# Kernel tuning notes

Hardware: AMD Instinct MI355X
Metric: run time of the kernel (lower is better)

Reference implementation:

```python
import jax, jax.numpy as jnp
import numpy as np

THETA = 10000.0
MASK_FILL = -60000.0

def _rope(x):
    # lucidrains rotary_embedding_torch semantics: interleaved pairs, full-dim rotation
    S, D = x.shape[-2], x.shape[-1]
    inv_freq = 1.0 / (THETA ** (jnp.arange(0, D, 2, dtype=jnp.float32) / D))  # [D/2]
    freqs = jnp.arange(S, dtype=jnp.float32)[:, None] * inv_freq[None, :]     # [S, D/2]
    freqs = jnp.repeat(freqs, 2, axis=-1)                                     # [S, D] (each freq twice)
    cos, sin = jnp.cos(freqs), jnp.sin(freqs)
    xr = x.reshape(x.shape[:-1] + (D // 2, 2))
    rot_half = jnp.stack((-xr[..., 1], xr[..., 0]), axis=-1).reshape(x.shape)  # (x1,x2)->(-x2,x1)
    return x * cos + rot_half * sin

def setup_inputs() -> dict:
    key = jax.random.key(0)
    kq, kk, kv, km = jax.random.split(key, 4)
    B, H, S, D = 4, 16, 2048, 128
    return {
        "query": jax.random.normal(kq, (B, H, S, D), dtype=jnp.float32),
        "key": jax.random.normal(kk, (B, H, S, D), dtype=jnp.float32),
        "value": jax.random.normal(kv, (B, H, S, D), dtype=jnp.float32),
        "mask": jax.random.randint(km, (1, 1, S, S), 0, 2, dtype=jnp.int32),
    }

def reference(query, key, value, mask):
    q = _rope(query)
    k = _rope(key)
    scale = 1.0 / jnp.sqrt(jnp.float32(q.shape[-1]))
    scores = jnp.einsum('bhqd,bhkd->bhqk', q, k) * scale
    scores = jnp.where(mask == 0, jnp.float32(MASK_FILL), scores)
    p_attn = jax.nn.softmax(scores, axis=-1)
    out = jnp.einsum('bhqk,bhkd->bhqd', p_attn, value)
    return out, p_attn
```

## Files before the change

### kernel.cpp

```cpp
#include <hip/hip_runtime.h>
#include <hip/hip_fp16.h>
#include <cstdint>
#include <cstddef>

#define Bn 4
#define Hn 16
#define Sn 2048
#define Dn 128
#define MSHIFT 8.0f

typedef _Float16 half8  __attribute__((ext_vector_type(8)));
typedef float    f32x16 __attribute__((ext_vector_type(16)));
typedef float    f32x4v __attribute__((ext_vector_type(4)));
typedef unsigned uint4v __attribute__((ext_vector_type(4)));

__device__ __forceinline__ int pk_f16(float a, float b){
  auto h = __builtin_amdgcn_cvt_pkrtz(a, b);
  return __builtin_bit_cast(int, h);
}


__global__ void k_rope_table(float2* __restrict__ tab){
  const int idx = blockIdx.x*256 + threadIdx.x;
  const int i = idx & 63, s = idx >> 6;
  const double invf = exp(-(double)i * (9.210340371976184 / 64.0));
  const double ang  = (double)s * invf;
  float2 cs; cs.x = (float)cos(ang); cs.y = (float)sin(ang);
  tab[idx] = cs;
}

__global__ void k_pack_qk(const float* __restrict__ q, const float* __restrict__ k,
                          const float2* __restrict__ tab,
                          half8* __restrict__ qp, half8* __restrict__ kp){
  const int t    = blockIdx.x*256 + threadIdx.x;
  const int lane = t & 63, ln = lane & 31, h = lane >> 5;
  const int dc   = (t >> 6) & 7;
  const int blk  = (t >> 9) & 63;
  const int bh   = t >> 15;
  const int s    = blk*32 + ln;
  const size_t roff = ((size_t)bh*Sn + s)*Dn + dc*16 + h*8;
  const float4 a0 = *(const float4*)(q + roff);
  const float4 a1 = *(const float4*)(q + roff + 4);
  const float4 b0 = *(const float4*)(k + roff);
  const float4 b1 = *(const float4*)(k + roff + 4);
  const float2* tb = tab + s*64 + dc*8 + h*4;
  const float2 c0 = tb[0], c1 = tb[1], c2 = tb[2], c3 = tb[3];
  const float SC = 0.08838834764831845f;
  half8 qo, ko;
  qo[0] = (_Float16)((a0.x*c0.x - a0.y*c0.y)*SC);
  qo[1] = (_Float16)((a0.y*c0.x + a0.x*c0.y)*SC);
  qo[2] = (_Float16)((a0.z*c1.x - a0.w*c1.y)*SC);
  qo[3] = (_Float16)((a0.w*c1.x + a0.z*c1.y)*SC);
  qo[4] = (_Float16)((a1.x*c2.x - a1.y*c2.y)*SC);
  qo[5] = (_Float16)((a1.y*c2.x + a1.x*c2.y)*SC);
  qo[6] = (_Float16)((a1.z*c3.x - a1.w*c3.y)*SC);
  qo[7] = (_Float16)((a1.w*c3.x + a1.z*c3.y)*SC);
  ko[0] = (_Float16)(b0.x*c0.x - b0.y*c0.y);
  ko[1] = (_Float16)(b0.y*c0.x + b0.x*c0.y);
  ko[2] = (_Float16)(b0.z*c1.x - b0.w*c1.y);
  ko[3] = (_Float16)(b0.w*c1.x + b0.z*c1.y);
  ko[4] = (_Float16)(b1.x*c2.x - b1.y*c2.y);
  ko[5] = (_Float16)(b1.y*c2.x + b1.x*c2.y);
  ko[6] = (_Float16)(b1.z*c3.x - b1.w*c3.y);
  ko[7] = (_Float16)(b1.w*c3.x + b1.z*c3.y);
  qp[t] = qo;
  kp[t] = ko;
}

__global__ void k_pack_v(const float* __restrict__ v, half8* __restrict__ vp){
  const int t    = blockIdx.x*256 + threadIdx.x;
  const int lane = t & 63, ln = lane & 31, h = lane >> 5;
  const int dt   = (t >> 6) & 3;
  const int k16  = (t >> 8) & 127;
  const int bh   = t >> 15;
  const size_t base = ((size_t)bh*Sn + k16*16 + h*8)*Dn + dt*32 + ln;
  half8 o;
#pragma unroll
  for (int j = 0; j < 8; ++j) o[j] = (_Float16)v[base + (size_t)j*Dn];
  vp[t] = o;
}

__global__ void k_maskbits(const int* __restrict__ mask, unsigned* __restrict__ mtb){
  const int g = blockIdx.x*256 + threadIdx.x;
  const int k = g & (Sn-1), q32 = g >> 11;
  unsigned bits = 0u;
  for (int j = 0; j < 32; ++j)
    bits |= (mask[(size_t)(q32*32 + j)*Sn + k] != 0 ? 1u : 0u) << j;
  mtb[g] = bits;
}


__global__ __launch_bounds__(512, 2) void attn_ps2(
    const half8* __restrict__ qp, const half8* __restrict__ kp,
    const unsigned* __restrict__ mtb, half8* __restrict__ wfrag,
    float* __restrict__ rinvb)
{
  const int bid  = blockIdx.x;
  const int work = ((bid & 7) << 6) + (bid >> 3);
  const int bh   = work >> 3;
  const int qg   = work & 7;
  const int w    = threadIdx.x >> 6;
  const int l    = threadIdx.x & 63;
  const int ln   = l & 31;
  const int h    = l >> 5;
  const int qb   = qg*8 + w;
  const int strip = bh*64 + qb;

  half8 qf[8];
#pragma unroll
  for (int dc = 0; dc < 8; ++dc)
    qf[dc] = qp[(((size_t)bh*64 + qb)*8 + dc)*64 + l];

  const unsigned* mrow = mtb + (size_t)qb*Sn;
  half8* wbase = wfrag + (size_t)strip*128*64;
  float L = 0.f;

  for (int kt = 0; kt < 64; ++kt){
    const half8* kf = kp + (((size_t)bh*64 + kt)*8)*64 + l;
    f32x16 a;
#pragma unroll
    for (int i = 0; i < 16; ++i) a[i] = 0.f;
#pragma unroll
    for (int dc = 0; dc < 8; ++dc)
      a = __builtin_amdgcn_mfma_f32_32x32x16_f16(kf[(size_t)dc*64], qf[dc], a, 0, 0, 0);

#pragma unroll
    for (int mm = 0; mm < 4; ++mm){
      const uint4v dw = *(const uint4v*)(mrow + kt*32 + mm*8 + h*4);
#pragma unroll
      for (int aa = 0; aa < 4; ++aa){
        const int r = mm*4 + aa;
        const float s = ((dw[aa] >> ln) & 1u) ? a[r] : -1.0e30f;
        const float u = __expf(s - MSHIFT);
        a[r] = u;
        L += u;
      }
    }

    int pk2[4][2];
#pragma unroll
    for (int b = 0; b < 4; ++b){
      pk2[b][0] = pk_f16(a[4*b+0], a[4*b+1]);
      pk2[b][1] = pk_f16(a[4*b+2], a[4*b+3]);
    }

#pragma unroll
    for (int t16 = 0; t16 < 2; ++t16){
      const int P00 = pk2[2*t16+0][0];
      const int P01 = pk2[2*t16+0][1];
      const int P10 = pk2[2*t16+1][0];
      const int P11 = pk2[2*t16+1][1];
      const int S00 = __shfl_xor(P00, 32, 64);
      const int S01 = __shfl_xor(P01, 32, 64);
      const int S10 = __shfl_xor(P10, 32, 64);
      const int S11 = __shfl_xor(P11, 32, 64);
      int4 bi;
      bi.x = h ? S10 : P00;
      bi.y = h ? S11 : P01;
      bi.z = h ? P10 : S00;
      bi.w = h ? P11 : S01;
      wbase[(size_t)(kt*2 + t16)*64 + l] = __builtin_bit_cast(half8, bi);
    }
  }

  L += __shfl_xor(L, 32, 64);
  if (l < 32) rinvb[(size_t)strip*32 + ln] = 1.0f / L;
}


__global__ __launch_bounds__(512, 2) void attn_o(
    const half8* __restrict__ vp, const half8* __restrict__ wfrag,
    const float* __restrict__ rinvb, float* __restrict__ out)
{
  __shared__ float pt[8][32][34];

  const int bid  = blockIdx.x;
  const int work = 511 - (((bid & 7) << 6) + (bid >> 3));
  const int bh   = work >> 3;
  const int qg   = work & 7;
  const int w    = threadIdx.x >> 6;
  const int l    = threadIdx.x & 63;
  const int ln   = l & 31;
  const int h    = l >> 5;
  const int qb   = qg*8 + w;
  const int strip = bh*64 + qb;

  f32x16 oacc[4];
#pragma unroll
  for (int dt = 0; dt < 4; ++dt)
#pragma unroll
    for (int i = 0; i < 16; ++i) oacc[dt][i] = 0.f;

  const half8* wbase = wfrag + (size_t)strip*128*64;
  const half8* vbase = vp + (size_t)bh*128*4*64;

#pragma unroll 4
  for (int ks = 0; ks < 128; ++ks){
    const half8 bf = wbase[(size_t)ks*64 + l];
    const half8* vf = vbase + (size_t)ks*4*64 + l;
#pragma unroll
    for (int dt = 0; dt < 4; ++dt)
      oacc[dt] = __builtin_amdgcn_mfma_f32_32x32x16_f16(vf[(size_t)dt*64], bf, oacc[dt], 0, 0, 0);
  }

  const float rinv = rinvb[(size_t)strip*32 + ln];
#pragma unroll
  for (int dt = 0; dt < 4; ++dt)
#pragma unroll
    for (int i = 0; i < 16; ++i) oacc[dt][i] *= rinv;

  const size_t obase = ((size_t)bh*Sn + qb*32)*Dn;
  const int rq = l >> 3;
  const int rc = (l & 7) * 4;
#pragma unroll
  for (int dt = 0; dt < 4; ++dt){
#pragma unroll
    for (int g = 0; g < 4; ++g){
      const int c = g*8 + h*4;
      float2 e0, e1;
      e0.x = oacc[dt][4*g+0]; e0.y = oacc[dt][4*g+1];
      e1.x = oacc[dt][4*g+2]; e1.y = oacc[dt][4*g+3];
      *(float2*)&pt[w][ln][c]   = e0;
      *(float2*)&pt[w][ln][c+2] = e1;
    }
#pragma unroll
    for (int i = 0; i < 4; ++i){
      const int qq = i*8 + rq;
      const float2 t0 = *(const float2*)&pt[w][qq][rc];
      const float2 t1 = *(const float2*)&pt[w][qq][rc+2];
      f32x4v o4; o4.x = t0.x; o4.y = t0.y; o4.z = t1.x; o4.w = t1.y;
      __builtin_nontemporal_store(o4, (f32x4v*)(out + obase + (size_t)qq*Dn + dt*32 + rc));
    }
  }
}


__global__ __launch_bounds__(512, 2) void k_expand(
    const half8* __restrict__ wfrag, const float* __restrict__ rinvb,
    float* __restrict__ pout)
{
  __shared__ _Float16 ps[32][1032];
  __shared__ float rv[32];

  const int b     = blockIdx.x;
  const int strip = b >> 1;
  const int hh    = b & 1;
  const int tid   = threadIdx.x;
  const int l     = tid & 63;
  const int w8    = tid >> 6;
  const int ln    = l & 31;
  const int h     = l >> 5;

  if (tid < 32) rv[tid] = rinvb[(size_t)strip*32 + tid];

#pragma unroll
  for (int i = 0; i < 8; ++i){
    const int cc = w8*8 + i;
    const half8 v = wfrag[((size_t)strip*128 + hh*64 + cc)*64 + l];
    *(half8*)&ps[ln][cc*16 + h*8] = v;
  }
  __syncthreads();

  const int bh = strip >> 6, qb = strip & 63;
  float* dst0 = pout + ((size_t)bh*Sn + qb*32)*Sn + hh*1024;
#pragma unroll
  for (int it = 0; it < 8; ++it){
    const int id  = it*512 + tid;
    const int row = id >> 7;
    const int c   = (id & 127) * 8;
    const half8 hv = *(const half8*)&ps[row][c];
    const float r = rv[row];
    f32x4v v0, v1;
    v0.x = (float)hv[0]*r; v0.y = (float)hv[1]*r; v0.z = (float)hv[2]*r; v0.w = (float)hv[3]*r;
    v1.x = (float)hv[4]*r; v1.y = (float)hv[5]*r; v1.z = (float)hv[6]*r; v1.w = (float)hv[7]*r;
    float* dp = dst0 + (size_t)row*Sn + c;
    __builtin_nontemporal_store(v0, (f32x4v*)dp);
    __builtin_nontemporal_store(v1, (f32x4v*)(dp + 4));
  }
}


extern "C" void kernel_launch(void* const* d_in, const int* in_sizes, int n_in,
                              void* d_out, int out_size, void* d_ws, size_t ws_size,
                              hipStream_t stream)
{
  const float* dq = (const float*)d_in[0];
  const float* dk = (const float*)d_in[1];
  const float* dv = (const float*)d_in[2];
  const int*   dm = (const int*)d_in[3];

  char* ws = (char*)d_ws;
  float2*   tab  = (float2*)ws;
  half8*    qp   = (half8*)(ws + (size_t)(1u<<20));
  half8*    kp   = (half8*)(ws + (size_t)(1u<<20) + ((size_t)32<<20));
  half8*    vp   = (half8*)(ws + (size_t)(1u<<20) + ((size_t)64<<20));
  unsigned* mtb  = (unsigned*)(ws + (size_t)(1u<<20) + ((size_t)96<<20));
  float*    rinvb= (float*)(ws + (size_t)(1u<<20) + ((size_t)97<<20));
  half8*    wfr  = (half8*)(ws + (size_t)(1u<<20) + ((size_t)98<<20));

  float* out  = (float*)d_out;
  float* pout = out + (size_t)Bn*Hn*Sn*Dn;

  k_rope_table<<<512,  256, 0, stream>>>(tab);
  k_pack_qk   <<<8192, 256, 0, stream>>>(dq, dk, tab, qp, kp);
  k_pack_v    <<<8192, 256, 0, stream>>>(dv, vp);
  k_maskbits  <<<512,  256, 0, stream>>>(dm, mtb);
  attn_ps2    <<<512,  512, 0, stream>>>(qp, kp, mtb, wfr, rinvb);
  attn_o      <<<512,  512, 0, stream>>>(vp, wfr, rinvb, out);
  k_expand    <<<8192, 512, 0, stream>>>(wfr, rinvb, pout);
}
```

Before: 1.033 ms.

## Fuse PV product into score kernel and merge rope-table with mask-bit prep

The P·V MFMA accumulation now runs inside the score kernel, using the fp16 probability fragments while they are still in registers. This removes the separate attn_o kernel and its re-read of the whole probability buffer. The rope-table and mask-bit kernels are merged into one launch with block-range dispatch, which saves a kernel launch. The cost is higher register pressure in the fused kernel (four extra 16-wide accumulators), which may reduce occupancy or cause spills under the 512x2 launch bounds.

```diff
diff --git a/kernel.cpp b/kernel.cpp
--- a/kernel.cpp
+++ b/kernel.cpp
@@ -20,13 +20,24 @@
 }
 
 
-__global__ void k_rope_table(float2* __restrict__ tab){
-  const int idx = blockIdx.x*256 + threadIdx.x;
-  const int i = idx & 63, s = idx >> 6;
-  const double invf = exp(-(double)i * (9.210340371976184 / 64.0));
-  const double ang  = (double)s * invf;
-  float2 cs; cs.x = (float)cos(ang); cs.y = (float)sin(ang);
-  tab[idx] = cs;
+__global__ void k_prep0(float2* __restrict__ tab,
+                        const int* __restrict__ mask, unsigned* __restrict__ mtb){
+  const int bid = blockIdx.x;
+  if (bid < 512){
+    const int idx = bid*256 + threadIdx.x;
+    const int i = idx & 63, s = idx >> 6;
+    const double invf = exp(-(double)i * (9.210340371976184 / 64.0));
+    const double ang  = (double)s * invf;
+    float2 cs; cs.x = (float)cos(ang); cs.y = (float)sin(ang);
+    tab[idx] = cs;
+  } else {
+    const int g = (bid - 512)*256 + threadIdx.x;
+    const int k = g & (Sn-1), q32 = g >> 11;
+    unsigned bits = 0u;
+    for (int j = 0; j < 32; ++j)
+      bits |= (mask[(size_t)(q32*32 + j)*Sn + k] != 0 ? 1u : 0u) << j;
+    mtb[g] = bits;
+  }
 }
 
 __global__ void k_pack_qk(const float* __restrict__ q, const float* __restrict__ k,
@@ -80,21 +91,15 @@
   vp[t] = o;
 }
 
-__global__ void k_maskbits(const int* __restrict__ mask, unsigned* __restrict__ mtb){
-  const int g = blockIdx.x*256 + threadIdx.x;
-  const int k = g & (Sn-1), q32 = g >> 11;
-  unsigned bits = 0u;
-  for (int j = 0; j < 32; ++j)
-    bits |= (mask[(size_t)(q32*32 + j)*Sn + k] != 0 ? 1u : 0u) << j;
-  mtb[g] = bits;
-}
-
-
-__global__ __launch_bounds__(512, 2) void attn_ps2(
+
+__global__ __launch_bounds__(512, 2) void attn_pvs(
     const half8* __restrict__ qp, const half8* __restrict__ kp,
-    const unsigned* __restrict__ mtb, half8* __restrict__ wfrag,
-    float* __restrict__ rinvb)
+    const half8* __restrict__ vp, const unsigned* __restrict__ mtb,
+    half8* __restrict__ wfrag, float* __restrict__ rinvb,
+    float* __restrict__ out)
 {
+  __shared__ float pt[8][32][34];
+
   const int bid  = blockIdx.x;
   const int work = ((bid & 7) << 6) + (bid >> 3);
   const int bh   = work >> 3;
@@ -111,7 +116,14 @@
   for (int dc = 0; dc < 8; ++dc)
     qf[dc] = qp[(((size_t)bh*64 + qb)*8 + dc)*64 + l];
 
+  f32x16 oacc[4];
+#pragma unroll
+  for (int dt = 0; dt < 4; ++dt)
+#pragma unroll
+    for (int i = 0; i < 16; ++i) oacc[dt][i] = 0.f;
+
   const unsigned* mrow = mtb + (size_t)qb*Sn;
+  const half8* vbase = vp + (size_t)bh*128*4*64;
   half8* wbase = wfrag + (size_t)strip*128*64;
   float L = 0.f;
 
@@ -159,51 +171,20 @@
       bi.y = h ? S11 : P01;
       bi.z = h ? P10 : S00;
       bi.w = h ? P11 : S01;
-      wbase[(size_t)(kt*2 + t16)*64 + l] = __builtin_bit_cast(half8, bi);
+      const half8 bf = __builtin_bit_cast(half8, bi);
+      const int ks = kt*2 + t16;
+      wbase[(size_t)ks*64 + l] = bf;
+      const half8* vf = vbase + (size_t)ks*4*64 + l;
+#pragma unroll
+      for (int dt = 0; dt < 4; ++dt)
+        oacc[dt] = __builtin_amdgcn_mfma_f32_32x32x16_f16(vf[(size_t)dt*64], bf, oacc[dt], 0, 0, 0);
     }
   }
 
   L += __shfl_xor(L, 32, 64);
-  if (l < 32) rinvb[(size_t)strip*32 + ln] = 1.0f / L;
-}
-
-
-__global__ __launch_bounds__(512, 2) void attn_o(
-    const half8* __restrict__ vp, const half8* __restrict__ wfrag,
-    const float* __restrict__ rinvb, float* __restrict__ out)
-{
-  __shared__ float pt[8][32][34];
-
-  const int bid  = blockIdx.x;
-  const int work = 511 - (((bid & 7) << 6) + (bid >> 3));
-  const int bh   = work >> 3;
-  const int qg   = work & 7;
-  const int w    = threadIdx.x >> 6;
-  const int l    = threadIdx.x & 63;
-  const int ln   = l & 31;
-  const int h    = l >> 5;
-  const int qb   = qg*8 + w;
-  const int strip = bh*64 + qb;
-
-  f32x16 oacc[4];
-#pragma unroll
-  for (int dt = 0; dt < 4; ++dt)
-#pragma unroll
-    for (int i = 0; i < 16; ++i) oacc[dt][i] = 0.f;
-
-  const half8* wbase = wfrag + (size_t)strip*128*64;
-  const half8* vbase = vp + (size_t)bh*128*4*64;
-
-#pragma unroll 4
-  for (int ks = 0; ks < 128; ++ks){
-    const half8 bf = wbase[(size_t)ks*64 + l];
-    const half8* vf = vbase + (size_t)ks*4*64 + l;
-#pragma unroll
-    for (int dt = 0; dt < 4; ++dt)
-      oacc[dt] = __builtin_amdgcn_mfma_f32_32x32x16_f16(vf[(size_t)dt*64], bf, oacc[dt], 0, 0, 0);
-  }
-
-  const float rinv = rinvb[(size_t)strip*32 + ln];
+  const float rinv = 1.0f / L;
+  if (l < 32) rinvb[(size_t)strip*32 + ln] = rinv;
+
 #pragma unroll
   for (int dt = 0; dt < 4; ++dt)
 #pragma unroll
@@ -301,11 +282,9 @@
   float* out  = (float*)d_out;
   float* pout = out + (size_t)Bn*Hn*Sn*Dn;
 
-  k_rope_table<<<512,  256, 0, stream>>>(tab);
+  k_prep0     <<<1024, 256, 0, stream>>>(tab, dm, mtb);
   k_pack_qk   <<<8192, 256, 0, stream>>>(dq, dk, tab, qp, kp);
   k_pack_v    <<<8192, 256, 0, stream>>>(dv, vp);
-  k_maskbits  <<<512,  256, 0, stream>>>(dm, mtb);
-  attn_ps2    <<<512,  512, 0, stream>>>(qp, kp, mtb, wfr, rinvb);
-  attn_o      <<<512,  512, 0, stream>>>(vp, wfr, rinvb, out);
+  attn_pvs    <<<512,  512, 0, stream>>>(qp, kp, vp, mtb, wfr, rinvb, out);
   k_expand    <<<8192, 512, 0, stream>>>(wfr, rinvb, pout);
 }
```

New measurement: 1.454 ms. 40.8% more time.

## Split score pass over key halves per wave and merge prep kernels

Applied to the files above, without the earlier changes.

The score/exp pass now gives each query strip to two waves, each covering half of the key tiles. Their partial row sums are combined through shared memory before the reciprocal is written, and the grid doubles to 1024 blocks. The rope-table and mask-bit kernels are merged into one launch to save a kernel boundary. The cost is an extra block-level sync and shared-memory reduction, and each block now loads Q fragments for four strips instead of eight.

```diff
diff --git a/kernel.cpp b/kernel.cpp
--- a/kernel.cpp
+++ b/kernel.cpp
@@ -20,13 +20,24 @@
 }
 
 
-__global__ void k_rope_table(float2* __restrict__ tab){
-  const int idx = blockIdx.x*256 + threadIdx.x;
-  const int i = idx & 63, s = idx >> 6;
-  const double invf = exp(-(double)i * (9.210340371976184 / 64.0));
-  const double ang  = (double)s * invf;
-  float2 cs; cs.x = (float)cos(ang); cs.y = (float)sin(ang);
-  tab[idx] = cs;
+__global__ void k_prep0(float2* __restrict__ tab,
+                        const int* __restrict__ mask, unsigned* __restrict__ mtb){
+  const int bid = blockIdx.x;
+  if (bid < 512){
+    const int idx = bid*256 + threadIdx.x;
+    const int i = idx & 63, s = idx >> 6;
+    const double invf = exp(-(double)i * (9.210340371976184 / 64.0));
+    const double ang  = (double)s * invf;
+    float2 cs; cs.x = (float)cos(ang); cs.y = (float)sin(ang);
+    tab[idx] = cs;
+  } else {
+    const int g = (bid - 512)*256 + threadIdx.x;
+    const int k = g & (Sn-1), q32 = g >> 11;
+    unsigned bits = 0u;
+    for (int j = 0; j < 32; ++j)
+      bits |= (mask[(size_t)(q32*32 + j)*Sn + k] != 0 ? 1u : 0u) << j;
+    mtb[g] = bits;
+  }
 }
 
 __global__ void k_pack_qk(const float* __restrict__ q, const float* __restrict__ k,
@@ -80,31 +91,25 @@
   vp[t] = o;
 }
 
-__global__ void k_maskbits(const int* __restrict__ mask, unsigned* __restrict__ mtb){
-  const int g = blockIdx.x*256 + threadIdx.x;
-  const int k = g & (Sn-1), q32 = g >> 11;
-  unsigned bits = 0u;
-  for (int j = 0; j < 32; ++j)
-    bits |= (mask[(size_t)(q32*32 + j)*Sn + k] != 0 ? 1u : 0u) << j;
-  mtb[g] = bits;
-}
-
-
-__global__ __launch_bounds__(512, 2) void attn_ps2(
+
+__global__ __launch_bounds__(512, 2) void attn_ps3(
     const half8* __restrict__ qp, const half8* __restrict__ kp,
     const unsigned* __restrict__ mtb, half8* __restrict__ wfrag,
     float* __restrict__ rinvb)
 {
+  __shared__ float redL[4][2][32];
+
   const int bid  = blockIdx.x;
-  const int work = ((bid & 7) << 6) + (bid >> 3);
-  const int bh   = work >> 3;
-  const int qg   = work & 7;
+  const int work = ((bid & 7) << 7) + (bid >> 3);
   const int w    = threadIdx.x >> 6;
   const int l    = threadIdx.x & 63;
   const int ln   = l & 31;
   const int h    = l >> 5;
-  const int qb   = qg*8 + w;
-  const int strip = bh*64 + qb;
+  const int sl   = w >> 1;
+  const int half = w & 1;
+  const int strip = work*4 + sl;
+  const int bh   = strip >> 6;
+  const int qb   = strip & 63;
 
   half8 qf[8];
 #pragma unroll
@@ -115,7 +120,8 @@
   half8* wbase = wfrag + (size_t)strip*128*64;
   float L = 0.f;
 
-  for (int kt = 0; kt < 64; ++kt){
+  const int kt0 = half*32;
+  for (int kt = kt0; kt < kt0 + 32; ++kt){
     const half8* kf = kp + (((size_t)bh*64 + kt)*8)*64 + l;
     f32x16 a;
 #pragma unroll
@@ -164,7 +170,12 @@
   }
 
   L += __shfl_xor(L, 32, 64);
-  if (l < 32) rinvb[(size_t)strip*32 + ln] = 1.0f / L;
+  if (l < 32) redL[sl][half][ln] = L;
+  __syncthreads();
+  if (half == 0 && l < 32){
+    const float Lt = redL[sl][0][ln] + redL[sl][1][ln];
+    rinvb[(size_t)strip*32 + ln] = 1.0f / Lt;
+  }
 }
 
 
@@ -301,11 +312,10 @@
   float* out  = (float*)d_out;
   float* pout = out + (size_t)Bn*Hn*Sn*Dn;
 
-  k_rope_table<<<512,  256, 0, stream>>>(tab);
+  k_prep0     <<<1024, 256, 0, stream>>>(tab, dm, mtb);
   k_pack_qk   <<<8192, 256, 0, stream>>>(dq, dk, tab, qp, kp);
   k_pack_v    <<<8192, 256, 0, stream>>>(dv, vp);
-  k_maskbits  <<<512,  256, 0, stream>>>(dm, mtb);
-  attn_ps2    <<<512,  512, 0, stream>>>(qp, kp, mtb, wfr, rinvb);
+  attn_ps3    <<<1024, 512, 0, stream>>>(qp, kp, mtb, wfr, rinvb);
   attn_o      <<<512,  512, 0, stream>>>(vp, wfr, rinvb, out);
   k_expand    <<<8192, 512, 0, stream>>>(wfr, rinvb, pout);
 }
```

Result: no change. 1.036 ms (+0.3%).
